# Kernel optimization log

Hardware: AMD Instinct MI355X
Metric: run time of the kernel (lower is better)

The kernel has to match this reference:

```python
import jax, jax.numpy as jnp
import numpy as np

B, L = 8, 1024
VOCAB = 5000
DW = 256            # d_word_vec = d_model
H = 3 * DW          # hidden_size = 768
NH, HD = 12, 64     # n_head, d_k
D = NH * HD         # 768 = nhead*head_dim
D_INNER = 3072
N_LAYERS = 2
N_HIDDEN = 1024
N_OUT = 5000
MASK = 0
SCALE = 1.0 / float(np.sqrt(HD))


def _sinusoid(n_pos, d_hid):
    pos = np.arange(n_pos, dtype=np.float64)[:, None]
    hid = np.arange(d_hid)[None, :]
    tab = pos / np.power(10000.0, 2 * (hid // 2) / d_hid)
    tab[:, 0::2] = np.sin(tab[:, 0::2])
    tab[:, 1::2] = np.cos(tab[:, 1::2])
    tab[0] = 0.0  # padding_idx=0
    return jnp.asarray(tab, dtype=jnp.float32)


def _ln(x, g, b, eps=1e-5):
    mu = x.mean(-1, keepdims=True)
    var = ((x - mu) ** 2).mean(-1, keepdims=True)
    return (x - mu) * jax.lax.rsqrt(var + eps) * g + b


def _dense(x, w, b):
    # w: [out, in] (torch Conv 1x1 / Linear convention)
    return jnp.einsum('...i,oi->...o', x, w) + b


def _pwff(x, w1, b1, w2, b2, g, bn):
    out = _dense(jax.nn.relu(_dense(x, w1, b1)), w2, b2)
    return _ln(out + x, g, bn)


def _msa1(x, relay, wq, bq, wk, bk, wv, bv, wo, bo):
    # x: [B, L, H] nodes, relay: [B, H]. Star-Transformer ring attention:
    # window = 3 local neighbors + the relay node (4 keys per query).
    Bx, Lx, _ = x.shape
    q = _dense(x, wq, bq).reshape(Bx, Lx, NH, HD)
    k = _dense(x, wk, bk).reshape(Bx, Lx, NH, HD)
    v = _dense(x, wv, bv).reshape(Bx, Lx, NH, HD)
    kp = jnp.pad(k, ((0, 0), (1, 1), (0, 0), (0, 0)))
    vp = jnp.pad(v, ((0, 0), (1, 1), (0, 0), (0, 0)))
    k_win = jnp.stack([kp[:, u:u + Lx] for u in range(3)], axis=2)  # [B,L,3,NH,HD]
    v_win = jnp.stack([vp[:, u:u + Lx] for u in range(3)], axis=2)
    rk = _dense(relay, wk, bk).reshape(Bx, NH, HD)
    rv = _dense(relay, wv, bv).reshape(Bx, NH, HD)
    s_loc = jnp.einsum('blnh,blwnh->blwn', q, k_win)
    s_rel = jnp.einsum('blnh,bnh->bln', q, rk)
    scores = jnp.concatenate([s_loc, s_rel[:, :, None, :]], axis=2) * SCALE  # [B,L,4,NH]
    a = jax.nn.softmax(scores, axis=2)
    att = jnp.einsum('blwn,blwnh->blnh', a[:, :, :3], v_win) + a[:, :, 3][..., None] * rv[:, None]
    return _dense(att.reshape(Bx, Lx, D), wo, bo)


def _msa2(relay, nodes, smask, wq, bq, wk, bk, wv, bv, wo, bo):
    # Satellite->planet global attention: single query (relay) over [relay; nodes].
    Bx = relay.shape[0]
    y = jnp.concatenate([relay[:, None, :], nodes], axis=1)  # [B, 1+L, H]
    q = _dense(relay, wq, bq).reshape(Bx, NH, HD)
    k = _dense(y, wk, bk).reshape(Bx, -1, NH, HD)
    v = _dense(y, wv, bv).reshape(Bx, -1, NH, HD)
    pre = jnp.einsum('bnh,bsnh->bns', q, k) * SCALE
    pre = jnp.where(smask[:, None, :], -jnp.inf, pre)
    a = jax.nn.softmax(pre, axis=2)
    att = jnp.einsum('bns,bsnh->bnh', a, v).reshape(Bx, D)
    return _dense(att, wo, bo)


def setup_inputs():
    ks = iter(jax.random.split(jax.random.key(0), 40))
    def w(shape):
        return jax.random.normal(next(ks), shape, dtype=jnp.float32) * 0.02
    def z(shape):
        return jnp.zeros(shape, jnp.float32)
    def o(shape):
        return jnp.ones(shape, jnp.float32)
    inp = {}
    inp['src_seq'] = jax.random.randint(next(ks), (B, L, 3), 0, VOCAB, dtype=jnp.int32)
    inp['positions'] = jax.random.randint(next(ks), (B,), 0, L, dtype=jnp.int32)
    inp['emb'] = w((VOCAB, DW))
    inp['pos_table'] = _sinusoid(L, H)
    inp['norm_g'] = o((N_LAYERS, H)); inp['norm_b'] = z((N_LAYERS, H))
    inp['pw_w1'] = w((N_LAYERS, D_INNER, H)); inp['pw_b1'] = z((N_LAYERS, D_INNER))
    inp['pw_w2'] = w((N_LAYERS, H, D_INNER)); inp['pw_b2'] = z((N_LAYERS, H))
    inp['pw_g'] = o((N_LAYERS, H)); inp['pw_bn'] = z((N_LAYERS, H))
    for p in ['ring', 'star']:
        inp[p + '_wq'] = w((N_LAYERS, D, H)); inp[p + '_bq'] = z((N_LAYERS, D))
        inp[p + '_wk'] = w((N_LAYERS, D, H)); inp[p + '_bk'] = z((N_LAYERS, D))
        inp[p + '_wv'] = w((N_LAYERS, D, H)); inp[p + '_bv'] = z((N_LAYERS, D))
        inp[p + '_wo'] = w((N_LAYERS, H, D)); inp[p + '_bo'] = z((N_LAYERS, H))
    inp['head_w1'] = w((3, N_HIDDEN, 2 * H)); inp['head_b1'] = z((3, N_HIDDEN))
    inp['head_w2'] = w((3, N_OUT, N_HIDDEN)); inp['head_b2'] = z((3, N_OUT))
    return inp


def reference(src_seq, positions, emb, pos_table, norm_g, norm_b, pw_w1, pw_b1, pw_w2, pw_b2, pw_g, pw_bn, ring_wq, ring_bq, ring_wk, ring_bk, ring_wv, ring_bv, ring_wo, ring_bo, star_wq, star_bq, star_wk, star_bk, star_wv, star_bv, star_wo, star_bo, head_w1, head_b1, head_w2, head_b2):
    Bx, Lx, _ = src_seq.shape
    # [B,L,3,DW] -> [B,L,H], add (frozen) sinusoid positional encoding
    x = emb[src_seq].reshape(Bx, Lx, H) + pos_table[None, :Lx]
    mask_pad = src_seq[:, :, 0] == MASK               # True at padded positions
    smask = jnp.concatenate([jnp.zeros((Bx, 1), bool), mask_pad], axis=1)
    nodes = x
    relay = x.mean(axis=1)                            # [B, H]
    for i in range(N_LAYERS):
        h = _pwff(nodes, pw_w1[i], pw_b1[i], pw_w2[i], pw_b2[i], pw_g[i], pw_bn[i])
        ring = _msa1(h, relay, ring_wq[i], ring_bq[i], ring_wk[i], ring_bk[i], ring_wv[i], ring_bv[i], ring_wo[i], ring_bo[i])
        nodes = jax.nn.leaky_relu(_ln(ring, norm_g[i], norm_b[i]))
        relay = jax.nn.leaky_relu(_msa2(relay, nodes, smask, star_wq[i], star_bq[i], star_wk[i], star_bk[i], star_wv[i], star_bv[i], star_wo[i], star_bo[i]))
        nodes = jnp.where(mask_pad[:, :, None], 0.0, nodes)
    target = nodes[jnp.arange(Bx), positions]         # [B, H]
    ft = jnp.concatenate([relay, target], axis=1)     # [B, 2H]
    outs = [_dense(jax.nn.relu(_dense(ft, head_w1[j], head_b1[j])), head_w2[j], head_b2[j]) for j in range(3)]
    return jnp.concatenate(outs, axis=1).reshape(3 * Bx, N_OUT)
```

## Files before the change

kernel.cpp:

```cpp
#include <hip/hip_runtime.h>
#include <cstdint>
#include <cstddef>


typedef unsigned short u16;
typedef __attribute__((ext_vector_type(4))) float f32x4;
typedef __attribute__((ext_vector_type(8))) __bf16 bf16x8;

#define NB 8
#define SEQ 1024
#define HDIM 768
#define NHEAD 12
#define HD 64
#define DINNER 3072
#define NHID 1024
#define NOUT 5000
#define ATT_SCALE 0.125f

static __device__ __forceinline__ float b2f(u16 u) {
  union { float f; uint32_t i; } v; v.i = ((uint32_t)u) << 16; return v.f;
}
static __device__ __forceinline__ u16 f2b(float f) {
  union { float f; uint32_t i; } v; v.f = f;
  uint32_t r = v.i + 0x7fffu + ((v.i >> 16) & 1u);
  return (u16)(r >> 16);
}
static __device__ __forceinline__ float2 b2f2(uint32_t u) {
  union { float f; uint32_t i; } lo, hi;
  lo.i = u << 16; hi.i = u & 0xffff0000u;
  return make_float2(lo.f, hi.f);
}

static __device__ __forceinline__ void gl2lds16(const void* g, void* l) {
  __builtin_amdgcn_global_load_lds(
      (__attribute__((address_space(1))) void*)(uintptr_t)g,
      (__attribute__((address_space(3))) void*)l, 16, 0, 0);
}

template <int N>
static __device__ __forceinline__ void wait_vmcnt() {
  if constexpr (N == 0) asm volatile("s_waitcnt vmcnt(0)" ::: "memory");
  else if constexpr (N == 4) asm volatile("s_waitcnt vmcnt(4)" ::: "memory");
  else if constexpr (N == 8) asm volatile("s_waitcnt vmcnt(8)" ::: "memory");
}

static __device__ __forceinline__ float blk_sum(float v, float* red) {
  #pragma unroll
  for (int off = 32; off > 0; off >>= 1) v += __shfl_down(v, off, 64);
  if ((threadIdx.x & 63) == 0) red[threadIdx.x >> 6] = v;
  __syncthreads();
  float r = red[0] + red[1] + red[2] + red[3];
  __syncthreads();
  return r;
}
static __device__ __forceinline__ float blk_max(float v, float* red) {
  #pragma unroll
  for (int off = 32; off > 0; off >>= 1) v = fmaxf(v, __shfl_down(v, off, 64));
  if ((threadIdx.x & 63) == 0) red[threadIdx.x >> 6] = v;
  __syncthreads();
  float r = fmaxf(fmaxf(red[0], red[1]), fmaxf(red[2], red[3]));
  __syncthreads();
  return r;
}

struct Cvt4 {
  const float* s0; const float* s1; const float* s2; const float* s3;
  u16* d0; u16* d1; u16* d2; u16* d3;
  int c1, c2, c3, c4;
};
__global__ __launch_bounds__(256) void cvt4_k(Cvt4 a) {
  const int i = blockIdx.x * 256 + threadIdx.x;
  if (i >= a.c4) return;
  const float* s; u16* d; int j;
  if (i < a.c1)      { s = a.s0; d = a.d0; j = i; }
  else if (i < a.c2) { s = a.s1; d = a.d1; j = i - a.c1; }
  else if (i < a.c3) { s = a.s2; d = a.d2; j = i - a.c2; }
  else               { s = a.s3; d = a.d3; j = i - a.c3; }
  const float4 v = ((const float4*)s)[j];
  ushort4 o;
  o.x = f2b(v.x); o.y = f2b(v.y); o.z = f2b(v.z); o.w = f2b(v.w);
  ((ushort4*)d)[j] = o;
}

__global__ __launch_bounds__(256) void zero_k(float4* __restrict__ p) {
  p[(size_t)blockIdx.x * 256 + threadIdx.x] = make_float4(0.f, 0.f, 0.f, 0.f);
}

template <int ACT, int SPLITK>
__global__ __launch_bounds__(256) void gemm_bt(
    const u16* __restrict__ A,
    const u16* W0, const u16* W1, const u16* W2,
    const float* b0, const float* b1, const float* b2,
    u16* C0, u16* C1, u16* C2,
    int M, int N, int K) {
  __shared__ u16 As[3][128 * 32];
  __shared__ u16 Bs[3][128 * 32];
  const int nblk = N >> 7;
  const int mat = (int)blockIdx.x / nblk;
  const u16* W = mat == 0 ? W0 : (mat == 1 ? W1 : W2);
  const float* bias = mat == 0 ? b0 : (mat == 1 ? b1 : b2);
  u16* C = mat == 0 ? C0 : (mat == 1 ? C1 : C2);

  const int tid  = threadIdx.x;
  const int wave = tid >> 6;
  const int lane = tid & 63;
  const int bm = blockIdx.y * 128;
  const int bn = ((int)blockIdx.x - mat * nblk) * 128;
  const int wrq = wave >> 1, wcq = wave & 1;
  const int r16 = lane & 15, quad = lane >> 4;
  const int srow = lane & 15;
  const int scol = (lane >> 4) << 3;

  const int Ks = K / SPLITK;
  const int kb = (int)blockIdx.z * Ks;
  const int nk = Ks >> 5;

  f32x4 acc[4][4] = {};

  auto STAGE = [&](int s, int t) {
    const int k0 = kb + (t << 5);
    #pragma unroll
    for (int q = 0; q < 2; ++q) {
      const int sub = wave * 2 + q;
      gl2lds16(A + (size_t)(bm + sub * 16 + srow) * K + (k0 + scol),
               (char*)&As[s][0] + (sub << 10));
      gl2lds16(W + (size_t)(bn + sub * 16 + srow) * K + (k0 + scol),
               (char*)&Bs[s][0] + (sub << 10));
    }
  };

  STAGE(0, 0);
  STAGE(1, 1);

  for (int t = 0; t < nk; ++t) {
    const int s = t % 3;
    if (t + 1 < nk) wait_vmcnt<4>(); else wait_vmcnt<0>();
    __builtin_amdgcn_s_barrier();
    __builtin_amdgcn_sched_barrier(0);
    bf16x8 af[4], bf[4];
    #pragma unroll
    for (int i = 0; i < 4; ++i)
      af[i] = *reinterpret_cast<const bf16x8*>(
          &As[s][((wrq * 4 + i) << 9) + (quad << 7) + (r16 << 3)]);
    #pragma unroll
    for (int j = 0; j < 4; ++j)
      bf[j] = *reinterpret_cast<const bf16x8*>(
          &Bs[s][((wcq * 4 + j) << 9) + (quad << 7) + (r16 << 3)]);
    if (t + 2 < nk) STAGE((t + 2) % 3, t + 2);
    __builtin_amdgcn_sched_barrier(0);
    #pragma unroll
    for (int i = 0; i < 4; ++i)
      #pragma unroll
      for (int j = 0; j < 4; ++j)
        acc[i][j] = __builtin_amdgcn_mfma_f32_16x16x32_bf16(af[i], bf[j], acc[i][j], 0, 0, 0);
  }

  #pragma unroll
  for (int j = 0; j < 4; ++j) {
    const int n = bn + wcq * 64 + j * 16 + r16;
    const float bv = bias[n];
    #pragma unroll
    for (int i = 0; i < 4; ++i) {
      const int m0 = bm + wrq * 64 + i * 16 + quad * 4;
      #pragma unroll
      for (int r = 0; r < 4; ++r) {
        float vv = acc[i][j][r];
        if (SPLITK == 1) {
          vv += bv;
          if (ACT == 1) vv = fmaxf(vv, 0.0f);
          C[(size_t)(m0 + r) * N + n] = f2b(vv);
        } else {
          if (blockIdx.z == 0) vv += bv;
          atomicAdd((float*)C + (size_t)(m0 + r) * N + n, vv);
        }
      }
    }
  }
}

__global__ __launch_bounds__(256) void embed_k(
    const int* __restrict__ src, const float* __restrict__ emb,
    const float* __restrict__ pt, float* __restrict__ x,
    u16* __restrict__ xb) {
  const int r = blockIdx.x;
  const int l = r & (SEQ - 1);
  const int tid = threadIdx.x;
  #pragma unroll
  for (int it = 0; it < 3; ++it) {
    const int idx = tid + it * 256;
    const int c = idx >> 8, d = idx & 255;
    const int tok = src[r * 3 + c];
    const float v = emb[(size_t)tok * 256 + d] + pt[(size_t)l * HDIM + idx];
    x[(size_t)r * HDIM + idx] = v;
    xb[(size_t)r * HDIM + idx] = f2b(v);
  }
}

__global__ __launch_bounds__(256) void relay_mean1_k(
    const float* __restrict__ x, float* __restrict__ part) {
  const int cg = blockIdx.x, seg = blockIdx.y, b = blockIdx.z;
  const int h = cg * 256 + threadIdx.x;
  float s = 0.f;
  const int l0 = seg * 64;
  for (int l = l0; l < l0 + 64; ++l) s += x[((size_t)b * SEQ + l) * HDIM + h];
  part[((size_t)b * 16 + seg) * HDIM + h] = s;
}
__global__ __launch_bounds__(256) void relay_mean2_k(
    const float* __restrict__ part, float* __restrict__ relay) {
  const int b = blockIdx.y;
  const int h = blockIdx.x * 256 + threadIdx.x;
  float s = 0.f;
  #pragma unroll
  for (int i = 0; i < 16; ++i) s += part[((size_t)b * 16 + i) * HDIM + h];
  relay[b * HDIM + h] = s * (1.0f / 1024.0f);
}

__global__ __launch_bounds__(256) void ln_resid_k(
    const float* __restrict__ pre, const float* __restrict__ res,
    const float* __restrict__ g, const float* __restrict__ bb,
    u16* __restrict__ out) {
  __shared__ float red[4];
  const int r = blockIdx.x;
  const int tid = threadIdx.x;
  const size_t base = (size_t)r * HDIM;
  float v0 = pre[base + tid]       + res[base + tid];
  float v1 = pre[base + tid + 256] + res[base + tid + 256];
  float v2 = pre[base + tid + 512] + res[base + tid + 512];
  const float mu = blk_sum(v0 + v1 + v2, red) * (1.0f / 768.0f);
  v0 -= mu; v1 -= mu; v2 -= mu;
  const float var = blk_sum(v0 * v0 + v1 * v1 + v2 * v2, red) * (1.0f / 768.0f);
  const float rs = rsqrtf(var + 1e-5f);
  out[base + tid]       = f2b(v0 * rs * g[tid]       + bb[tid]);
  out[base + tid + 256] = f2b(v1 * rs * g[tid + 256] + bb[tid + 256]);
  out[base + tid + 512] = f2b(v2 * rs * g[tid + 512] + bb[tid + 512]);
}

__global__ __launch_bounds__(256) void ln_leaky_mask_k(
    const float* __restrict__ pre, const float* __restrict__ g,
    const float* __restrict__ bb, const int* __restrict__ src,
    float* __restrict__ out, u16* __restrict__ outb) {
  __shared__ float red[4];
  const int r = blockIdx.x;
  const int tid = threadIdx.x;
  const size_t base = (size_t)r * HDIM;
  float v0 = pre[base + tid];
  float v1 = pre[base + tid + 256];
  float v2 = pre[base + tid + 512];
  const float mu = blk_sum(v0 + v1 + v2, red) * (1.0f / 768.0f);
  v0 -= mu; v1 -= mu; v2 -= mu;
  const float var = blk_sum(v0 * v0 + v1 * v1 + v2 * v2, red) * (1.0f / 768.0f);
  const float rs = rsqrtf(var + 1e-5f);
  const bool masked = (src[r * 3] == 0);
  float y0 = v0 * rs * g[tid]       + bb[tid];
  float y1 = v1 * rs * g[tid + 256] + bb[tid + 256];
  float y2 = v2 * rs * g[tid + 512] + bb[tid + 512];
  y0 = y0 > 0.f ? y0 : 0.01f * y0;
  y1 = y1 > 0.f ? y1 : 0.01f * y1;
  y2 = y2 > 0.f ? y2 : 0.01f * y2;
  if (masked) { y0 = 0.f; y1 = 0.f; y2 = 0.f; }
  out[base + tid]       = y0;  outb[base + tid]       = f2b(y0);
  out[base + tid + 256] = y1;  outb[base + tid + 256] = f2b(y1);
  out[base + tid + 512] = y2;  outb[base + tid + 512] = f2b(y2);
}

__global__ __launch_bounds__(256) void ring_attn_k(
    const u16* __restrict__ q, const u16* __restrict__ k,
    const u16* __restrict__ v, const float* __restrict__ rk,
    const float* __restrict__ rv, u16* __restrict__ att) {
  __shared__ float qs[HDIM];
  __shared__ float aw[NHEAD][4];
  const int r = blockIdx.x;
  const int b = r >> 10, l = r & (SEQ - 1);
  const int tid = threadIdx.x;
  const size_t base = (size_t)r * HDIM;
  #pragma unroll
  for (int it = 0; it < 3; ++it) {
    const int idx = tid + it * 256;
    qs[idx] = b2f(q[base + idx]);
  }
  __syncthreads();
  if (tid < 192) {
    const int u_ = tid >> 2;
    const int l4 = tid & 3;
    const int n = u_ >> 2, w = u_ & 3;
    const float* qrow = qs + n * HD + l4 * 16;
    float a = 0.f;
    if (w < 3) {
      const int ll = l - 1 + w;
      if (ll >= 0 && ll < SEQ) {
        const uint4* kp4 =
            (const uint4*)(k + base + (size_t)(w - 1) * HDIM + n * HD + l4 * 16);
        #pragma unroll
        for (int t = 0; t < 2; ++t) {
          const uint4 u = kp4[t];
          const float2 f0 = b2f2(u.x), f1 = b2f2(u.y);
          const float2 f2_ = b2f2(u.z), f3 = b2f2(u.w);
          const float* q8 = qrow + t * 8;
          a += q8[0] * f0.x + q8[1] * f0.y + q8[2] * f1.x + q8[3] * f1.y
             + q8[4] * f2_.x + q8[5] * f2_.y + q8[6] * f3.x + q8[7] * f3.y;
        }
      }
    } else {
      const float4* kp4 = (const float4*)(rk + b * HDIM + n * HD + l4 * 16);
      #pragma unroll
      for (int t = 0; t < 4; ++t) {
        const float4 kv = kp4[t];
        const float* q4 = qrow + t * 4;
        a += q4[0] * kv.x + q4[1] * kv.y + q4[2] * kv.z + q4[3] * kv.w;
      }
    }
    a += __shfl_xor(a, 1, 4);
    a += __shfl_xor(a, 2, 4);
    if (l4 == 0) aw[n][w] = a * ATT_SCALE;
  }
  __syncthreads();
  if (tid < NHEAD) {
    const float s0 = aw[tid][0], s1 = aw[tid][1], s2 = aw[tid][2], s3 = aw[tid][3];
    const float m = fmaxf(fmaxf(s0, s1), fmaxf(s2, s3));
    const float e0 = __expf(s0 - m), e1 = __expf(s1 - m);
    const float e2 = __expf(s2 - m), e3 = __expf(s3 - m);
    const float inv = 1.0f / (e0 + e1 + e2 + e3);
    aw[tid][0] = e0 * inv; aw[tid][1] = e1 * inv;
    aw[tid][2] = e2 * inv; aw[tid][3] = e3 * inv;
  }
  __syncthreads();
  #pragma unroll
  for (int it = 0; it < 3; ++it) {
    const int idx = tid + it * 256;
    const int n = idx >> 6;
    float acc = aw[n][3] * rv[b * HDIM + idx];
    if (l > 0)       acc += aw[n][0] * b2f(v[base - HDIM + idx]);
    acc += aw[n][1] * b2f(v[base + idx]);
    if (l < SEQ - 1) acc += aw[n][2] * b2f(v[base + HDIM + idx]);
    att[base + idx] = f2b(acc);
  }
}

__global__ __launch_bounds__(256) void msa2_attn_k(
    const float* __restrict__ q2, const float* __restrict__ rk2,
    const float* __restrict__ rv2, const u16* __restrict__ k2,
    const u16* __restrict__ v2, const int* __restrict__ src,
    float* __restrict__ att) {
  __shared__ float qs[HD];
  __shared__ float sc[SEQ + 1];
  __shared__ float red[4];
  __shared__ float vred[4][HD];
  const int bid = blockIdx.x;
  const int b = bid / NHEAD, n = bid % NHEAD;
  const int tid = threadIdx.x;
  const int hb = b * HDIM + n * HD;
  if (tid < HD) qs[tid] = q2[hb + tid];
  __syncthreads();
  float lmax = -1e30f;
  for (int s = tid; s <= SEQ; s += 256) {
    float sco;
    if (s == 0) {
      float a = 0.f;
      #pragma unroll
      for (int d = 0; d < HD; ++d) a += qs[d] * rk2[hb + d];
      sco = a * ATT_SCALE;
    } else {
      const int l = s - 1;
      if (src[(b * SEQ + l) * 3] == 0) {
        sco = -1e30f;
      } else {
        const uint4* kp4 =
            (const uint4*)(k2 + ((size_t)b * SEQ + l) * HDIM + n * HD);
        float a = 0.f;
        #pragma unroll
        for (int t = 0; t < 8; ++t) {
          const uint4 u = kp4[t];
          const float2 f0 = b2f2(u.x), f1 = b2f2(u.y);
          const float2 f2_ = b2f2(u.z), f3 = b2f2(u.w);
          const float* q8 = qs + t * 8;
          a += q8[0] * f0.x + q8[1] * f0.y + q8[2] * f1.x + q8[3] * f1.y
             + q8[4] * f2_.x + q8[5] * f2_.y + q8[6] * f3.x + q8[7] * f3.y;
        }
        sco = a * ATT_SCALE;
      }
    }
    sc[s] = sco;
    lmax = fmaxf(lmax, sco);
  }
  lmax = blk_max(lmax, red);
  float lsum = 0.f;
  for (int s = tid; s <= SEQ; s += 256) {
    const float e = __expf(sc[s] - lmax);
    sc[s] = e;
    lsum += e;
  }
  lsum = blk_sum(lsum, red);
  {
    const int dd = tid & 63, grp = tid >> 6;
    float acc = 0.f;
    const u16* vp = v2 + (size_t)b * SEQ * HDIM + n * HD + dd;
    for (int l = grp; l < SEQ; l += 4)
      acc += sc[l + 1] * b2f(vp[(size_t)l * HDIM]);
    vred[grp][dd] = acc;
  }
  __syncthreads();
  if (tid < HD) {
    const float inv = 1.0f / lsum;
    const float a = sc[0] * rv2[hb + tid]
                  + vred[0][tid] + vred[1][tid] + vred[2][tid] + vred[3][tid];
    att[hb + tid] = a * inv;
  }
}

__global__ __launch_bounds__(256) void relay_proj_k(
    const float* __restrict__ A, int N, int nm,
    const float* W0, const float* W1, const float* W2,
    const float* b0, const float* b1, const float* b2v,
    float* O0, float* O1, float* O2, int act) {
  const int wid = blockIdx.x * 4 + (threadIdx.x >> 6);
  const int lane = threadIdx.x & 63;
  const int mat = wid / N, n = wid % N;
  const float* W  = mat == 0 ? W0 : (mat == 1 ? W1 : W2);
  const float* bb = mat == 0 ? b0 : (mat == 1 ? b1 : b2v);
  float* O        = mat == 0 ? O0 : (mat == 1 ? O1 : O2);
  const float4* wr = (const float4*)(W + (size_t)n * HDIM);
  float acc[NB] = {};
  #pragma unroll
  for (int it = 0; it < 3; ++it) {
    const int k4 = it * 64 + lane;
    const float4 wv = wr[k4];
    #pragma unroll
    for (int b = 0; b < NB; ++b) {
      const float4 av = *(const float4*)&A[b * HDIM + k4 * 4];
      acc[b] += av.x * wv.x + av.y * wv.y + av.z * wv.z + av.w * wv.w;
    }
  }
  #pragma unroll
  for (int b = 0; b < NB; ++b) {
    float a = acc[b];
    #pragma unroll
    for (int off = 32; off > 0; off >>= 1) a += __shfl_down(a, off, 64);
    if (lane == 0) {
      float v = a + bb[n];
      if (act == 2) v = v > 0.f ? v : 0.01f * v;
      O[(size_t)b * N + n] = v;
    }
  }
}

__global__ __launch_bounds__(256) void ft_k(
    const float* __restrict__ relay, const float* __restrict__ nodes,
    const int* __restrict__ positions, float* __restrict__ ft) {
  const int gid = blockIdx.x * 256 + threadIdx.x;
  const int b = gid / 1536, j = gid % 1536;
  if (j < HDIM) {
    ft[gid] = relay[b * HDIM + j];
  } else {
    const int p = positions[b];
    ft[gid] = nodes[((size_t)b * SEQ + p) * HDIM + (j - HDIM)];
  }
}

__global__ __launch_bounds__(256) void head1_k(
    const float* __restrict__ ft, const float* __restrict__ w,
    const float* __restrict__ bias, float* __restrict__ hid) {
  __shared__ float fs[NB * 1536];
  const int j = blockIdx.y;
  {
    const float4* s4 = (const float4*)ft;
    float4* d4 = (float4*)fs;
    for (int i = threadIdx.x; i < (NB * 1536) / 4; i += 256) d4[i] = s4[i];
  }
  __syncthreads();
  const int wave = threadIdx.x >> 6, lane = threadIdx.x & 63;
  const int o = blockIdx.x * 4 + wave;
  const float4* wr = (const float4*)(w + ((size_t)j * NHID + o) * 1536);
  float acc[NB] = {};
  #pragma unroll
  for (int it = 0; it < 6; ++it) {
    const int k4 = it * 64 + lane;
    const float4 wv = wr[k4];
    #pragma unroll
    for (int b = 0; b < NB; ++b) {
      const float4 hv = *(const float4*)&fs[b * 1536 + k4 * 4];
      acc[b] += hv.x * wv.x + hv.y * wv.y + hv.z * wv.z + hv.w * wv.w;
    }
  }
  #pragma unroll
  for (int b = 0; b < NB; ++b) {
    float a = acc[b];
    #pragma unroll
    for (int off = 32; off > 0; off >>= 1) a += __shfl_down(a, off, 64);
    if (lane == 0)
      hid[((size_t)j * NB + b) * NHID + o] = fmaxf(a + bias[j * NHID + o], 0.f);
  }
}

__global__ __launch_bounds__(256) void head2_k(
    const float* __restrict__ hid, const float* __restrict__ w,
    const float* __restrict__ bias, float* __restrict__ out) {
  __shared__ float hs[NB * NHID];
  const int j = blockIdx.y;
  {
    const float4* s4 = (const float4*)(hid + (size_t)j * NB * NHID);
    float4* d4 = (float4*)hs;
    for (int i = threadIdx.x; i < (NB * NHID) / 4; i += 256) d4[i] = s4[i];
  }
  __syncthreads();
  const int wave = threadIdx.x >> 6, lane = threadIdx.x & 63;
  const int o = blockIdx.x * 4 + wave;
  const float4* wr = (const float4*)(w + ((size_t)j * NOUT + o) * NHID);
  float acc[NB] = {};
  #pragma unroll
  for (int it = 0; it < 4; ++it) {
    const int k4 = it * 64 + lane;
    const float4 wv = wr[k4];
    #pragma unroll
    for (int b = 0; b < NB; ++b) {
      const float4 hv = *(const float4*)&hs[b * NHID + k4 * 4];
      acc[b] += hv.x * wv.x + hv.y * wv.y + hv.z * wv.z + hv.w * wv.w;
    }
  }
  #pragma unroll
  for (int b = 0; b < NB; ++b) {
    float a = acc[b];
    #pragma unroll
    for (int off = 32; off > 0; off >>= 1) a += __shfl_down(a, off, 64);
    if (lane == 0)
      out[(size_t)(b * 3 + j) * NOUT + o] = a + bias[j * NOUT + o];
  }
}

extern "C" void kernel_launch(void* const* d_in, const int* in_sizes, int n_in,
                              void* d_out, int out_size, void* d_ws, size_t ws_size,
                              hipStream_t stream) {
  (void)in_sizes; (void)n_in; (void)out_size; (void)ws_size;
  const int* src       = (const int*)d_in[0];
  const int* positions = (const int*)d_in[1];
  const float* emb   = (const float*)d_in[2];
  const float* pt    = (const float*)d_in[3];
  const float* norm_g = (const float*)d_in[4]; const float* norm_b = (const float*)d_in[5];
  const float* pw_w1 = (const float*)d_in[6];  const float* pw_b1 = (const float*)d_in[7];
  const float* pw_w2 = (const float*)d_in[8];  const float* pw_b2 = (const float*)d_in[9];
  const float* pw_g  = (const float*)d_in[10]; const float* pw_bn = (const float*)d_in[11];
  const float* ring_wq = (const float*)d_in[12]; const float* ring_bq = (const float*)d_in[13];
  const float* ring_wk = (const float*)d_in[14]; const float* ring_bk = (const float*)d_in[15];
  const float* ring_wv = (const float*)d_in[16]; const float* ring_bv = (const float*)d_in[17];
  const float* ring_wo = (const float*)d_in[18]; const float* ring_bo = (const float*)d_in[19];
  const float* star_wq = (const float*)d_in[20]; const float* star_bq = (const float*)d_in[21];
  const float* star_wk = (const float*)d_in[22]; const float* star_bk = (const float*)d_in[23];
  const float* star_wv = (const float*)d_in[24]; const float* star_bv = (const float*)d_in[25];
  const float* star_wo = (const float*)d_in[26]; const float* star_bo = (const float*)d_in[27];
  const float* head_w1 = (const float*)d_in[28]; const float* head_b1 = (const float*)d_in[29];
  const float* head_w2 = (const float*)d_in[30]; const float* head_b2 = (const float*)d_in[31];

  char* ws = (char*)d_ws;
  const size_t NTOK = (size_t)NB * SEQ * HDIM;
  const size_t U = NTOK * 2;
  float* nodes   = (float*)(ws);
  u16* inner     = (u16*)(ws + 2 * U);
  float* prefA   = (float*)(ws + 6 * U);
  u16* hbuf      = (u16*)(ws + 2 * U);
  u16* qb        = (u16*)(ws + 3 * U);
  u16* kb        = (u16*)(ws + 4 * U);
  u16* vb        = (u16*)(ws + 5 * U);
  u16* attb      = (u16*)(ws + 6 * U);
  float* prefB   = (float*)(ws + 2 * U);
  u16* nodes_b16 = (u16*)(ws + 7 * U);
  u16* k2b       = (u16*)(ws + 4 * U);
  u16* v2b       = (u16*)(ws + 5 * U);
  u16* wc        = (u16*)(ws + 8 * U);
  char* small    = ws + 8 * U + 9437184;
  float* part  = (float*)(small);
  float* relay = (float*)(small + 393216);
  float* sb0 = (float*)(small + 393216 + 1 * 24576);
  float* sb1 = (float*)(small + 393216 + 2 * 24576);
  float* sb2 = (float*)(small + 393216 + 3 * 24576);
  float* sb3 = (float*)(small + 393216 + 4 * 24576);
  float* ftb = (float*)(small + 393216 + 5 * 24576);
  float* hid = (float*)(small + 393216 + 5 * 24576 + 49152);

  embed_k<<<NB * SEQ, 256, 0, stream>>>(src, emb, pt, nodes, nodes_b16);
  relay_mean1_k<<<dim3(3, 16, NB), 256, 0, stream>>>(nodes, part);
  relay_mean2_k<<<dim3(3, NB), 256, 0, stream>>>(part, relay);

  const int NW1 = DINNER * HDIM;
  const int NQK = HDIM * HDIM;
  const int M = NB * SEQ;

  for (int i = 0; i < 2; ++i) {
    const float* pw_w1_l = pw_w1 + (size_t)i * NW1;
    const float* pw_w2_l = pw_w2 + (size_t)i * NW1;
    const float* pw_b1_l = pw_b1 + (size_t)i * DINNER;
    const float* pw_b2_l = pw_b2 + (size_t)i * HDIM;
    const float* pw_g_l  = pw_g + (size_t)i * HDIM;
    const float* pw_bn_l = pw_bn + (size_t)i * HDIM;
    const float* ng_l = norm_g + (size_t)i * HDIM;
    const float* nb_l = norm_b + (size_t)i * HDIM;
    const float* rwq = ring_wq + (size_t)i * NQK; const float* rbq = ring_bq + (size_t)i * HDIM;
    const float* rwk = ring_wk + (size_t)i * NQK; const float* rbk = ring_bk + (size_t)i * HDIM;
    const float* rwv = ring_wv + (size_t)i * NQK; const float* rbv = ring_bv + (size_t)i * HDIM;
    const float* rwo = ring_wo + (size_t)i * NQK; const float* rbo = ring_bo + (size_t)i * HDIM;
    const float* swq = star_wq + (size_t)i * NQK; const float* sbq = star_bq + (size_t)i * HDIM;
    const float* swk = star_wk + (size_t)i * NQK; const float* sbk = star_bk + (size_t)i * HDIM;
    const float* swv = star_wv + (size_t)i * NQK; const float* sbv = star_bv + (size_t)i * HDIM;
    const float* swo = star_wo + (size_t)i * NQK; const float* sbo = star_bo + (size_t)i * HDIM;

    u16* wc_pw1 = wc;
    u16* wc_pw2 = wc + NW1;
    {
      Cvt4 a = { pw_w1_l, pw_w2_l, pw_w1_l, pw_w1_l,
                 wc_pw1, wc_pw2, wc_pw1, wc_pw1,
                 NW1 / 4, NW1 / 2, NW1 / 2, NW1 / 2 };
      cvt4_k<<<(NW1 / 2 + 255) / 256, 256, 0, stream>>>(a);
    }
    gemm_bt<1, 1><<<dim3(DINNER / 128, M / 128, 1), 256, 0, stream>>>(
        nodes_b16, wc_pw1, wc_pw1, wc_pw1, pw_b1_l, pw_b1_l, pw_b1_l,
        inner, inner, inner, M, DINNER, HDIM);
    zero_k<<<(int)(NTOK / 1024), 256, 0, stream>>>((float4*)prefA);
    gemm_bt<0, 2><<<dim3(HDIM / 128, M / 128, 2), 256, 0, stream>>>(
        inner, wc_pw2, wc_pw2, wc_pw2, pw_b2_l, pw_b2_l, pw_b2_l,
        (u16*)prefA, (u16*)prefA, (u16*)prefA, M, HDIM, DINNER);
    ln_resid_k<<<M, 256, 0, stream>>>(prefA, nodes, pw_g_l, pw_bn_l, hbuf);

    u16* wc_rq = wc;
    u16* wc_rk = wc + NQK;
    u16* wc_rv = wc + 2 * NQK;
    u16* wc_ro = wc + 3 * NQK;
    {
      Cvt4 a = { rwq, rwk, rwv, rwo, wc_rq, wc_rk, wc_rv, wc_ro,
                 NQK / 4, NQK / 2, 3 * NQK / 4, NQK };
      cvt4_k<<<(NQK + 255) / 256, 256, 0, stream>>>(a);
    }
    gemm_bt<0, 1><<<dim3(3 * (HDIM / 128), M / 128, 1), 256, 0, stream>>>(
        hbuf, wc_rq, wc_rk, wc_rv, rbq, rbk, rbv,
        qb, kb, vb, M, HDIM, HDIM);
    relay_proj_k<<<2 * HDIM / 4, 256, 0, stream>>>(
        relay, HDIM, 2, rwk, rwv, rwk, rbk, rbv, rbk, sb0, sb1, sb2, 0);
    ring_attn_k<<<NB * SEQ, 256, 0, stream>>>(qb, kb, vb, sb0, sb1, attb);
    zero_k<<<(int)(NTOK / 1024), 256, 0, stream>>>((float4*)prefB);
    gemm_bt<0, 2><<<dim3(HDIM / 128, M / 128, 2), 256, 0, stream>>>(
        attb, wc_ro, wc_ro, wc_ro, rbo, rbo, rbo,
        (u16*)prefB, (u16*)prefB, (u16*)prefB, M, HDIM, HDIM);
    ln_leaky_mask_k<<<M, 256, 0, stream>>>(prefB, ng_l, nb_l, src, nodes, nodes_b16);

    u16* wc_sk = wc;
    u16* wc_sv = wc + NQK;
    {
      Cvt4 a = { swk, swv, swk, swk, wc_sk, wc_sv, wc_sk, wc_sk,
                 NQK / 4, NQK / 2, NQK / 2, NQK / 2 };
      cvt4_k<<<(NQK / 2 + 255) / 256, 256, 0, stream>>>(a);
    }
    gemm_bt<0, 1><<<dim3(2 * (HDIM / 128), M / 128, 1), 256, 0, stream>>>(
        nodes_b16, wc_sk, wc_sv, wc_sv, sbk, sbv, sbv,
        k2b, v2b, v2b, M, HDIM, HDIM);
    relay_proj_k<<<3 * HDIM / 4, 256, 0, stream>>>(
        relay, HDIM, 3, swq, swk, swv, sbq, sbk, sbv, sb0, sb1, sb2, 0);
    msa2_attn_k<<<NB * NHEAD, 256, 0, stream>>>(sb0, sb1, sb2, k2b, v2b, src, sb3);
    relay_proj_k<<<HDIM / 4, 256, 0, stream>>>(
        sb3, HDIM, 1, swo, swo, swo, sbo, sbo, sbo, relay, sb1, sb2, 2);
  }

  ft_k<<<48, 256, 0, stream>>>(relay, nodes, positions, ftb);
  head1_k<<<dim3(NHID / 4, 3), 256, 0, stream>>>(ftb, head_w1, head_b1, hid);
  head2_k<<<dim3(NOUT / 4, 3), 256, 0, stream>>>(hid, head_w2, head_b2, (float*)d_out);
}
```

Baseline: 1.273 ms.

## Load GEMM A operand directly to registers, add TM tile, drop split-K atomics

The GEMM now stages only the weight tile in LDS and loads the activation operand straight from global memory into registers, double-buffered across k-steps. The kernel is templated on M-tile height (128 or 64), and split-K with atomic float accumulation is replaced by smaller M tiles that write bf16 directly. This removes the zeroing kernels and the fp32 atomics, and the layer-norm kernels now read bf16 pre-activations. In exchange, A reads are no longer shared through LDS, so they become uncoalesced per-lane global loads. Rounding the pre-norm sums to bf16 also costs precision.

After: 1.474 ms. 1.16x slower.

```diff
diff --git a/kernel.cpp b/kernel.cpp
--- a/kernel.cpp
+++ b/kernel.cpp
@@ -41,6 +41,7 @@
 static __device__ __forceinline__ void wait_vmcnt() {
   if constexpr (N == 0) asm volatile("s_waitcnt vmcnt(0)" ::: "memory");
   else if constexpr (N == 4) asm volatile("s_waitcnt vmcnt(4)" ::: "memory");
+  else if constexpr (N == 6) asm volatile("s_waitcnt vmcnt(6)" ::: "memory");
   else if constexpr (N == 8) asm volatile("s_waitcnt vmcnt(8)" ::: "memory");
 }
 
@@ -82,18 +83,14 @@
   ((ushort4*)d)[j] = o;
 }
 
-__global__ __launch_bounds__(256) void zero_k(float4* __restrict__ p) {
-  p[(size_t)blockIdx.x * 256 + threadIdx.x] = make_float4(0.f, 0.f, 0.f, 0.f);
-}
-
-template <int ACT, int SPLITK>
+template <int ACT, int TM>
 __global__ __launch_bounds__(256) void gemm_bt(
     const u16* __restrict__ A,
     const u16* W0, const u16* W1, const u16* W2,
     const float* b0, const float* b1, const float* b2,
     u16* C0, u16* C1, u16* C2,
     int M, int N, int K) {
-  __shared__ u16 As[3][128 * 32];
+  constexpr int MI = TM / 32;
   __shared__ u16 Bs[3][128 * 32];
   const int nblk = N >> 7;
   const int mat = (int)blockIdx.x / nblk;
@@ -104,75 +101,81 @@
   const int tid  = threadIdx.x;
   const int wave = tid >> 6;
   const int lane = tid & 63;
-  const int bm = blockIdx.y * 128;
+  const int bm = blockIdx.y * TM;
   const int bn = ((int)blockIdx.x - mat * nblk) * 128;
   const int wrq = wave >> 1, wcq = wave & 1;
   const int r16 = lane & 15, quad = lane >> 4;
-  const int srow = lane & 15;
-  const int scol = (lane >> 4) << 3;
-
-  const int Ks = K / SPLITK;
-  const int kb = (int)blockIdx.z * Ks;
-  const int nk = Ks >> 5;
-
-  f32x4 acc[4][4] = {};
+
+  const int nk = K >> 5;
+
+  f32x4 acc[MI][4] = {};
 
   auto STAGE = [&](int s, int t) {
-    const int k0 = kb + (t << 5);
+    const int k0 = t << 5;
     #pragma unroll
     for (int q = 0; q < 2; ++q) {
       const int sub = wave * 2 + q;
-      gl2lds16(A + (size_t)(bm + sub * 16 + srow) * K + (k0 + scol),
-               (char*)&As[s][0] + (sub << 10));
-      gl2lds16(W + (size_t)(bn + sub * 16 + srow) * K + (k0 + scol),
+      gl2lds16(W + (size_t)(bn + sub * 16 + r16) * K + (k0 + (quad << 3)),
                (char*)&Bs[s][0] + (sub << 10));
     }
   };
 
+#define LOADA(AF_, T_)                                                       \
+  {                                                                          \
+    _Pragma("unroll")                                                        \
+    for (int i_ = 0; i_ < MI; ++i_)                                          \
+      (AF_)[i_] = *reinterpret_cast<const bf16x8*>(                          \
+          A + (size_t)(bm + wrq * (TM / 2) + i_ * 16 + r16) * K              \
+            + (((T_) << 5) + (quad << 3)));                                  \
+  }
+
+#define GSTEP(S_, AFC_, AFN_, TN_, TS_)                                      \
+  {                                                                          \
+    wait_vmcnt<MI + 2>();                                                    \
+    __builtin_amdgcn_s_barrier();                                            \
+    __builtin_amdgcn_sched_barrier(0);                                       \
+    bf16x8 bf[4];                                                            \
+    _Pragma("unroll")                                                        \
+    for (int j_ = 0; j_ < 4; ++j_)                                           \
+      bf[j_] = *reinterpret_cast<const bf16x8*>(                             \
+          &Bs[S_][((wcq * 4 + j_) << 9) + (quad << 7) + (r16 << 3)]);        \
+    if ((TS_) < nk) STAGE((TS_) % 3, (TS_));                                 \
+    __builtin_amdgcn_sched_barrier(0);                                       \
+    if ((TN_) < nk) LOADA(AFN_, (TN_));                                      \
+    __builtin_amdgcn_sched_barrier(0);                                       \
+    _Pragma("unroll")                                                        \
+    for (int i_ = 0; i_ < MI; ++i_)                                          \
+      _Pragma("unroll")                                                      \
+      for (int j_ = 0; j_ < 4; ++j_)                                         \
+        acc[i_][j_] = __builtin_amdgcn_mfma_f32_16x16x32_bf16(               \
+            (AFC_)[i_], bf[j_], acc[i_][j_], 0, 0, 0);                       \
+  }
+
+  bf16x8 afa[MI], afb[MI];
   STAGE(0, 0);
   STAGE(1, 1);
-
-  for (int t = 0; t < nk; ++t) {
-    const int s = t % 3;
-    if (t + 1 < nk) wait_vmcnt<4>(); else wait_vmcnt<0>();
-    __builtin_amdgcn_s_barrier();
-    __builtin_amdgcn_sched_barrier(0);
-    bf16x8 af[4], bf[4];
-    #pragma unroll
-    for (int i = 0; i < 4; ++i)
-      af[i] = *reinterpret_cast<const bf16x8*>(
-          &As[s][((wrq * 4 + i) << 9) + (quad << 7) + (r16 << 3)]);
-    #pragma unroll
-    for (int j = 0; j < 4; ++j)
-      bf[j] = *reinterpret_cast<const bf16x8*>(
-          &Bs[s][((wcq * 4 + j) << 9) + (quad << 7) + (r16 << 3)]);
-    if (t + 2 < nk) STAGE((t + 2) % 3, t + 2);
-    __builtin_amdgcn_sched_barrier(0);
-    #pragma unroll
-    for (int i = 0; i < 4; ++i)
-      #pragma unroll
-      for (int j = 0; j < 4; ++j)
-        acc[i][j] = __builtin_amdgcn_mfma_f32_16x16x32_bf16(af[i], bf[j], acc[i][j], 0, 0, 0);
-  }
+  __builtin_amdgcn_sched_barrier(0);
+  LOADA(afa, 0);
+
+  for (int t = 0; t < nk; t += 2) {
+    GSTEP(t % 3, afa, afb, t + 1, t + 2);
+    GSTEP((t + 1) % 3, afb, afa, t + 2, t + 3);
+  }
+#undef GSTEP
+#undef LOADA
 
   #pragma unroll
   for (int j = 0; j < 4; ++j) {
     const int n = bn + wcq * 64 + j * 16 + r16;
     const float bv = bias[n];
     #pragma unroll
-    for (int i = 0; i < 4; ++i) {
-      const int m0 = bm + wrq * 64 + i * 16 + quad * 4;
+    for (int i = 0; i < MI; ++i) {
+      const int m0 = bm + wrq * (TM / 2) + i * 16 + quad * 4;
       #pragma unroll
       for (int r = 0; r < 4; ++r) {
-        float vv = acc[i][j][r];
-        if (SPLITK == 1) {
-          vv += bv;
-          if (ACT == 1) vv = fmaxf(vv, 0.0f);
-          C[(size_t)(m0 + r) * N + n] = f2b(vv);
-        } else {
-          if (blockIdx.z == 0) vv += bv;
-          atomicAdd((float*)C + (size_t)(m0 + r) * N + n, vv);
-        }
+        float vv = acc[i][j][r] + bv;
+        if (ACT == 1) vv = fmaxf(vv, 0.0f);
+        C[(size_t)(m0 + r) * N + n] = f2b(vv);
       }
     }
   }
@@ -216,16 +219,16 @@
 }
 
 __global__ __launch_bounds__(256) void ln_resid_k(
-    const float* __restrict__ pre, const float* __restrict__ res,
+    const u16* __restrict__ pre, const float* __restrict__ res,
     const float* __restrict__ g, const float* __restrict__ bb,
     u16* __restrict__ out) {
   __shared__ float red[4];
   const int r = blockIdx.x;
   const int tid = threadIdx.x;
   const size_t base = (size_t)r * HDIM;
-  float v0 = pre[base + tid]       + res[base + tid];
-  float v1 = pre[base + tid + 256] + res[base + tid + 256];
-  float v2 = pre[base + tid + 512] + res[base + tid + 512];
+  float v0 = b2f(pre[base + tid])       + res[base + tid];
+  float v1 = b2f(pre[base + tid + 256]) + res[base + tid + 256];
+  float v2 = b2f(pre[base + tid + 512]) + res[base + tid + 512];
   const float mu = blk_sum(v0 + v1 + v2, red) * (1.0f / 768.0f);
   v0 -= mu; v1 -= mu; v2 -= mu;
   const float var = blk_sum(v0 * v0 + v1 * v1 + v2 * v2, red) * (1.0f / 768.0f);
@@ -236,16 +239,16 @@
 }
 
 __global__ __launch_bounds__(256) void ln_leaky_mask_k(
-    const float* __restrict__ pre, const float* __restrict__ g,
+    const u16* __restrict__ pre, const float* __restrict__ g,
     const float* __restrict__ bb, const int* __restrict__ src,
     float* __restrict__ out, u16* __restrict__ outb) {
   __shared__ float red[4];
   const int r = blockIdx.x;
   const int tid = threadIdx.x;
   const size_t base = (size_t)r * HDIM;
-  float v0 = pre[base + tid];
-  float v1 = pre[base + tid + 256];
-  float v2 = pre[base + tid + 512];
+  float v0 = b2f(pre[base + tid]);
+  float v1 = b2f(pre[base + tid + 256]);
+  float v2 = b2f(pre[base + tid + 512]);
   const float mu = blk_sum(v0 + v1 + v2, red) * (1.0f / 768.0f);
   v0 -= mu; v1 -= mu; v2 -= mu;
   const float var = blk_sum(v0 * v0 + v1 * v1 + v2 * v2, red) * (1.0f / 768.0f);
@@ -554,13 +557,13 @@
   const size_t U = NTOK * 2;
   float* nodes   = (float*)(ws);
   u16* inner     = (u16*)(ws + 2 * U);
-  float* prefA   = (float*)(ws + 6 * U);
+  u16* prelnA    = (u16*)(ws + 6 * U);
   u16* hbuf      = (u16*)(ws + 2 * U);
   u16* qb        = (u16*)(ws + 3 * U);
   u16* kb        = (u16*)(ws + 4 * U);
   u16* vb        = (u16*)(ws + 5 * U);
   u16* attb      = (u16*)(ws + 6 * U);
-  float* prefB   = (float*)(ws + 2 * U);
+  u16* prelnB    = (u16*)(ws + 3 * U);
   u16* nodes_b16 = (u16*)(ws + 7 * U);
   u16* k2b       = (u16*)(ws + 4 * U);
   u16* v2b       = (u16*)(ws + 5 * U);
@@ -609,14 +612,13 @@
                  NW1 / 4, NW1 / 2, NW1 / 2, NW1 / 2 };
       cvt4_k<<<(NW1 / 2 + 255) / 256, 256, 0, stream>>>(a);
     }
-    gemm_bt<1, 1><<<dim3(DINNER / 128, M / 128, 1), 256, 0, stream>>>(
+    gemm_bt<1, 128><<<dim3(DINNER / 128, M / 128), 256, 0, stream>>>(
         nodes_b16, wc_pw1, wc_pw1, wc_pw1, pw_b1_l, pw_b1_l, pw_b1_l,
         inner, inner, inner, M, DINNER, HDIM);
-    zero_k<<<(int)(NTOK / 1024), 256, 0, stream>>>((float4*)prefA);
-    gemm_bt<0, 2><<<dim3(HDIM / 128, M / 128, 2), 256, 0, stream>>>(
+    gemm_bt<0, 64><<<dim3(HDIM / 128, M / 64), 256, 0, stream>>>(
         inner, wc_pw2, wc_pw2, wc_pw2, pw_b2_l, pw_b2_l, pw_b2_l,
-        (u16*)prefA, (u16*)prefA, (u16*)prefA, M, HDIM, DINNER);
-    ln_resid_k<<<M, 256, 0, stream>>>(prefA, nodes, pw_g_l, pw_bn_l, hbuf);
+        prelnA, prelnA, prelnA, M, HDIM, DINNER);
+    ln_resid_k<<<M, 256, 0, stream>>>(prelnA, nodes, pw_g_l, pw_bn_l, hbuf);
 
     u16* wc_rq = wc;
     u16* wc_rk = wc + NQK;
@@ -627,17 +629,16 @@
                  NQK / 4, NQK / 2, 3 * NQK / 4, NQK };
       cvt4_k<<<(NQK + 255) / 256, 256, 0, stream>>>(a);
     }
-    gemm_bt<0, 1><<<dim3(3 * (HDIM / 128), M / 128, 1), 256, 0, stream>>>(
+    gemm_bt<0, 64><<<dim3(3 * (HDIM / 128), M / 64), 256, 0, stream>>>(
         hbuf, wc_rq, wc_rk, wc_rv, rbq, rbk, rbv,
         qb, kb, vb, M, HDIM, HDIM);
     relay_proj_k<<<2 * HDIM / 4, 256, 0, stream>>>(
         relay, HDIM, 2, rwk, rwv, rwk, rbk, rbv, rbk, sb0, sb1, sb2, 0);
     ring_attn_k<<<NB * SEQ, 256, 0, stream>>>(qb, kb, vb, sb0, sb1, attb);
-    zero_k<<<(int)(NTOK / 1024), 256, 0, stream>>>((float4*)prefB);
-    gemm_bt<0, 2><<<dim3(HDIM / 128, M / 128, 2), 256, 0, stream>>>(
+    gemm_bt<0, 64><<<dim3(HDIM / 128, M / 64), 256, 0, stream>>>(
         attb, wc_ro, wc_ro, wc_ro, rbo, rbo, rbo,
-        (u16*)prefB, (u16*)prefB, (u16*)prefB, M, HDIM, HDIM);
-    ln_leaky_mask_k<<<M, 256, 0, stream>>>(prefB, ng_l, nb_l, src, nodes, nodes_b16);
+        prelnB, prelnB, prelnB, M, HDIM, HDIM);
+    ln_leaky_mask_k<<<M, 256, 0, stream>>>(prelnB, ng_l, nb_l, src, nodes, nodes_b16);
 
     u16* wc_sk = wc;
     u16* wc_sv = wc + NQK;
@@ -646,7 +647,7 @@
                  NQK / 4, NQK / 2, NQK / 2, NQK / 2 };
       cvt4_k<<<(NQK / 2 + 255) / 256, 256, 0, stream>>>(a);
     }
-    gemm_bt<0, 1><<<dim3(2 * (HDIM / 128), M / 128, 1), 256, 0, stream>>>(
+    gemm_bt<0, 64><<<dim3(2 * (HDIM / 128), M / 64), 256, 0, stream>>>(
         nodes_b16, wc_sk, wc_sv, wc_sv, sbk, sbv, sbv,
         k2b, v2b, v2b, M, HDIM, HDIM);
     relay_proj_k<<<3 * HDIM / 4, 256, 0, stream>>>(
```

## Remove split-K atomics and remap GEMM tiles to XCDs for L2 reuse

Applied to the files above, without the earlier changes.

Drops the split-K fp32 atomicAdd path and its zeroing kernels, so every GEMM writes its output once in bf16 and the following LayerNorm kernels read bf16. The GEMM grid becomes 1D, with blocks spread across the 8 XCDs so that each XCD owns a contiguous range of M tiles and shares A rows in its own L2. This removes atomic traffic and the zero launches but rounds the pre-LayerNorm sums to bf16. It also halves the number of blocks for the K=3072 GEMM, which lengthens each block's K loop.

New measurement: 1.142 ms. -10.3%, faster.

```diff
diff --git a/kernel.cpp b/kernel.cpp
--- a/kernel.cpp
+++ b/kernel.cpp
@@ -82,11 +82,7 @@
   ((ushort4*)d)[j] = o;
 }
 
-__global__ __launch_bounds__(256) void zero_k(float4* __restrict__ p) {
-  p[(size_t)blockIdx.x * 256 + threadIdx.x] = make_float4(0.f, 0.f, 0.f, 0.f);
-}
-
-template <int ACT, int SPLITK>
+template <int ACT, int ORDER>
 __global__ __launch_bounds__(256) void gemm_bt(
     const u16* __restrict__ A,
     const u16* W0, const u16* W1, const u16* W2,
@@ -96,7 +92,17 @@
   __shared__ u16 As[3][128 * 32];
   __shared__ u16 Bs[3][128 * 32];
   const int nblk = N >> 7;
-  const int mat = (int)blockIdx.x / nblk;
+  const int mpx = (M >> 7) >> 3;
+  const int J = (int)gridDim.x >> 3;
+  const int NXB = J / mpx;
+  const int o = (int)blockIdx.x;
+  const int xcd = o & 7, j = o >> 3;
+  int lp, n;
+  if (ORDER == 0) { lp = j / NXB; n = j - lp * NXB; }
+  else            { n = j / mpx;  lp = j - n * mpx; }
+  const int bm = (xcd * mpx + lp) << 7;
+  const int mat = n / nblk;
+  const int bn = (n - mat * nblk) << 7;
   const u16* W = mat == 0 ? W0 : (mat == 1 ? W1 : W2);
   const float* bias = mat == 0 ? b0 : (mat == 1 ? b1 : b2);
   u16* C = mat == 0 ? C0 : (mat == 1 ? C1 : C2);
@@ -104,27 +110,21 @@
   const int tid  = threadIdx.x;
   const int wave = tid >> 6;
   const int lane = tid & 63;
-  const int bm = blockIdx.y * 128;
-  const int bn = ((int)blockIdx.x - mat * nblk) * 128;
   const int wrq = wave >> 1, wcq = wave & 1;
   const int r16 = lane & 15, quad = lane >> 4;
-  const int srow = lane & 15;
-  const int scol = (lane >> 4) << 3;
-
-  const int Ks = K / SPLITK;
-  const int kb = (int)blockIdx.z * Ks;
-  const int nk = Ks >> 5;
+
+  const int nk = K >> 5;
 
   f32x4 acc[4][4] = {};
 
   auto STAGE = [&](int s, int t) {
-    const int k0 = kb + (t << 5);
+    const int k0 = t << 5;
     #pragma unroll
     for (int q = 0; q < 2; ++q) {
       const int sub = wave * 2 + q;
-      gl2lds16(A + (size_t)(bm + sub * 16 + srow) * K + (k0 + scol),
+      gl2lds16(A + (size_t)(bm + sub * 16 + r16) * K + (k0 + (quad << 3)),
                (char*)&As[s][0] + (sub << 10));
-      gl2lds16(W + (size_t)(bn + sub * 16 + srow) * K + (k0 + scol),
+      gl2lds16(W + (size_t)(bn + sub * 16 + r16) * K + (k0 + (quad << 3)),
                (char*)&Bs[s][0] + (sub << 10));
     }
   };
@@ -143,36 +143,30 @@
       af[i] = *reinterpret_cast<const bf16x8*>(
           &As[s][((wrq * 4 + i) << 9) + (quad << 7) + (r16 << 3)]);
     #pragma unroll
-    for (int j = 0; j < 4; ++j)
-      bf[j] = *reinterpret_cast<const bf16x8*>(
-          &Bs[s][((wcq * 4 + j) << 9) + (quad << 7) + (r16 << 3)]);
+    for (int j_ = 0; j_ < 4; ++j_)
+      bf[j_] = *reinterpret_cast<const bf16x8*>(
+          &Bs[s][((wcq * 4 + j_) << 9) + (quad << 7) + (r16 << 3)]);
     if (t + 2 < nk) STAGE((t + 2) % 3, t + 2);
     __builtin_amdgcn_sched_barrier(0);
     #pragma unroll
     for (int i = 0; i < 4; ++i)
       #pragma unroll
-      for (int j = 0; j < 4; ++j)
-        acc[i][j] = __builtin_amdgcn_mfma_f32_16x16x32_bf16(af[i], bf[j], acc[i][j], 0, 0, 0);
-  }
-
-  #pragma unroll
-  for (int j = 0; j < 4; ++j) {
-    const int n = bn + wcq * 64 + j * 16 + r16;
-    const float bv = bias[n];
+      for (int j_ = 0; j_ < 4; ++j_)
+        acc[i][j_] = __builtin_amdgcn_mfma_f32_16x16x32_bf16(af[i], bf[j_], acc[i][j_], 0, 0, 0);
+  }
+
+  #pragma unroll
+  for (int j_ = 0; j_ < 4; ++j_) {
+    const int nn = bn + wcq * 64 + j_ * 16 + r16;
+    const float bv = bias[nn];
     #pragma unroll
     for (int i = 0; i < 4; ++i) {
       const int m0 = bm + wrq * 64 + i * 16 + quad * 4;
       #pragma unroll
       for (int r = 0; r < 4; ++r) {
-        float vv = acc[i][j][r];
-        if (SPLITK == 1) {
-          vv += bv;
-          if (ACT == 1) vv = fmaxf(vv, 0.0f);
-          C[(size_t)(m0 + r) * N + n] = f2b(vv);
-        } else {
-          if (blockIdx.z == 0) vv += bv;
-          atomicAdd((float*)C + (size_t)(m0 + r) * N + n, vv);
-        }
+        float vv = acc[i][j_][r] + bv;
+        if (ACT == 1) vv = fmaxf(vv, 0.0f);
+        C[(size_t)(m0 + r) * N + nn] = f2b(vv);
       }
     }
   }
@@ -216,16 +210,16 @@
 }
 
 __global__ __launch_bounds__(256) void ln_resid_k(
-    const float* __restrict__ pre, const float* __restrict__ res,
+    const u16* __restrict__ pre, const float* __restrict__ res,
     const float* __restrict__ g, const float* __restrict__ bb,
     u16* __restrict__ out) {
   __shared__ float red[4];
   const int r = blockIdx.x;
   const int tid = threadIdx.x;
   const size_t base = (size_t)r * HDIM;
-  float v0 = pre[base + tid]       + res[base + tid];
-  float v1 = pre[base + tid + 256] + res[base + tid + 256];
-  float v2 = pre[base + tid + 512] + res[base + tid + 512];
+  float v0 = b2f(pre[base + tid])       + res[base + tid];
+  float v1 = b2f(pre[base + tid + 256]) + res[base + tid + 256];
+  float v2 = b2f(pre[base + tid + 512]) + res[base + tid + 512];
   const float mu = blk_sum(v0 + v1 + v2, red) * (1.0f / 768.0f);
   v0 -= mu; v1 -= mu; v2 -= mu;
   const float var = blk_sum(v0 * v0 + v1 * v1 + v2 * v2, red) * (1.0f / 768.0f);
@@ -236,16 +230,16 @@
 }
 
 __global__ __launch_bounds__(256) void ln_leaky_mask_k(
-    const float* __restrict__ pre, const float* __restrict__ g,
+    const u16* __restrict__ pre, const float* __restrict__ g,
     const float* __restrict__ bb, const int* __restrict__ src,
     float* __restrict__ out, u16* __restrict__ outb) {
   __shared__ float red[4];
   const int r = blockIdx.x;
   const int tid = threadIdx.x;
   const size_t base = (size_t)r * HDIM;
-  float v0 = pre[base + tid];
-  float v1 = pre[base + tid + 256];
-  float v2 = pre[base + tid + 512];
+  float v0 = b2f(pre[base + tid]);
+  float v1 = b2f(pre[base + tid + 256]);
+  float v2 = b2f(pre[base + tid + 512]);
   const float mu = blk_sum(v0 + v1 + v2, red) * (1.0f / 768.0f);
   v0 -= mu; v1 -= mu; v2 -= mu;
   const float var = blk_sum(v0 * v0 + v1 * v1 + v2 * v2, red) * (1.0f / 768.0f);
@@ -554,13 +548,13 @@
   const size_t U = NTOK * 2;
   float* nodes   = (float*)(ws);
   u16* inner     = (u16*)(ws + 2 * U);
-  float* prefA   = (float*)(ws + 6 * U);
+  u16* prelnA    = (u16*)(ws + 6 * U);
   u16* hbuf      = (u16*)(ws + 2 * U);
   u16* qb        = (u16*)(ws + 3 * U);
   u16* kb        = (u16*)(ws + 4 * U);
   u16* vb        = (u16*)(ws + 5 * U);
   u16* attb      = (u16*)(ws + 6 * U);
-  float* prefB   = (float*)(ws + 2 * U);
+  u16* prelnB    = (u16*)(ws + 3 * U);
   u16* nodes_b16 = (u16*)(ws + 7 * U);
   u16* k2b       = (u16*)(ws + 4 * U);
   u16* v2b       = (u16*)(ws + 5 * U);
@@ -582,6 +576,7 @@
   const int NW1 = DINNER * HDIM;
   const int NQK = HDIM * HDIM;
   const int M = NB * SEQ;
+  const int MP = M / 128;
 
   for (int i = 0; i < 2; ++i) {
     const float* pw_w1_l = pw_w1 + (size_t)i * NW1;
@@ -609,14 +604,13 @@
                  NW1 / 4, NW1 / 2, NW1 / 2, NW1 / 2 };
       cvt4_k<<<(NW1 / 2 + 255) / 256, 256, 0, stream>>>(a);
     }
-    gemm_bt<1, 1><<<dim3(DINNER / 128, M / 128, 1), 256, 0, stream>>>(
+    gemm_bt<1, 1><<<(DINNER / 128) * MP, 256, 0, stream>>>(
         nodes_b16, wc_pw1, wc_pw1, wc_pw1, pw_b1_l, pw_b1_l, pw_b1_l,
         inner, inner, inner, M, DINNER, HDIM);
-    zero_k<<<(int)(NTOK / 1024), 256, 0, stream>>>((float4*)prefA);
-    gemm_bt<0, 2><<<dim3(HDIM / 128, M / 128, 2), 256, 0, stream>>>(
+    gemm_bt<0, 0><<<(HDIM / 128) * MP, 256, 0, stream>>>(
         inner, wc_pw2, wc_pw2, wc_pw2, pw_b2_l, pw_b2_l, pw_b2_l,
-        (u16*)prefA, (u16*)prefA, (u16*)prefA, M, HDIM, DINNER);
-    ln_resid_k<<<M, 256, 0, stream>>>(prefA, nodes, pw_g_l, pw_bn_l, hbuf);
+        prelnA, prelnA, prelnA, M, HDIM, DINNER);
+    ln_resid_k<<<M, 256, 0, stream>>>(prelnA, nodes, pw_g_l, pw_bn_l, hbuf);
 
     u16* wc_rq = wc;
     u16* wc_rk = wc + NQK;
@@ -627,17 +621,16 @@
                  NQK / 4, NQK / 2, 3 * NQK / 4, NQK };
       cvt4_k<<<(NQK + 255) / 256, 256, 0, stream>>>(a);
     }
-    gemm_bt<0, 1><<<dim3(3 * (HDIM / 128), M / 128, 1), 256, 0, stream>>>(
+    gemm_bt<0, 0><<<3 * (HDIM / 128) * MP, 256, 0, stream>>>(
         hbuf, wc_rq, wc_rk, wc_rv, rbq, rbk, rbv,
         qb, kb, vb, M, HDIM, HDIM);
     relay_proj_k<<<2 * HDIM / 4, 256, 0, stream>>>(
         relay, HDIM, 2, rwk, rwv, rwk, rbk, rbv, rbk, sb0, sb1, sb2, 0);
     ring_attn_k<<<NB * SEQ, 256, 0, stream>>>(qb, kb, vb, sb0, sb1, attb);
-    zero_k<<<(int)(NTOK / 1024), 256, 0, stream>>>((float4*)prefB);
-    gemm_bt<0, 2><<<dim3(HDIM / 128, M / 128, 2), 256, 0, stream>>>(
+    gemm_bt<0, 0><<<(HDIM / 128) * MP, 256, 0, stream>>>(
         attb, wc_ro, wc_ro, wc_ro, rbo, rbo, rbo,
-        (u16*)prefB, (u16*)prefB, (u16*)prefB, M, HDIM, HDIM);
-    ln_leaky_mask_k<<<M, 256, 0, stream>>>(prefB, ng_l, nb_l, src, nodes, nodes_b16);
+        prelnB, prelnB, prelnB, M, HDIM, HDIM);
+    ln_leaky_mask_k<<<M, 256, 0, stream>>>(prelnB, ng_l, nb_l, src, nodes, nodes_b16);
 
     u16* wc_sk = wc;
     u16* wc_sv = wc + NQK;
@@ -646,7 +639,7 @@
                  NQK / 4, NQK / 2, NQK / 2, NQK / 2 };
       cvt4_k<<<(NQK / 2 + 255) / 256, 256, 0, stream>>>(a);
     }
-    gemm_bt<0, 1><<<dim3(2 * (HDIM / 128), M / 128, 1), 256, 0, stream>>>(
+    gemm_bt<0, 0><<<2 * (HDIM / 128) * MP, 256, 0, stream>>>(
         nodes_b16, wc_sk, wc_sv, wc_sv, sbk, sbv, sbv,
         k2b, v2b, v2b, M, HDIM, HDIM);
     relay_proj_k<<<3 * HDIM / 4, 256, 0, stream>>>(
```
